# Kernel tuning notes

Measured on AMD Instinct MI355X. Metric: run time of the kernel, lower is better.

The kernel has to match this reference:

```python
import jax, jax.numpy as jnp
import numpy as np

N_NODES = 100000
N_EDGES = 640000
IN_DIM = 128
HID_DIM = 256
N_CLASS = 40
K = 3  # propagation steps


def setup_inputs() -> dict:
    key = jax.random.key(0)
    ks = jax.random.split(key, 5)
    feats = jax.random.normal(ks[0], (N_NODES, IN_DIM), dtype=jnp.float32)
    src = jax.random.randint(ks[1], (N_EDGES,), 0, N_NODES, dtype=jnp.int32)
    dst = jax.random.randint(ks[2], (N_EDGES,), 0, N_NODES, dtype=jnp.int32)
    W1 = jax.random.normal(ks[3], (IN_DIM, HID_DIM), dtype=jnp.float32) * (1.0 / np.sqrt(IN_DIM))
    b1 = jnp.zeros((HID_DIM,), dtype=jnp.float32)
    W2 = jax.random.normal(ks[4], (HID_DIM, N_CLASS), dtype=jnp.float32) * (1.0 / np.sqrt(HID_DIM))
    b2 = jnp.zeros((N_CLASS,), dtype=jnp.float32)
    return {"feats": feats, "src": src, "dst": dst, "W1": W1, "b1": b1, "W2": W2, "b2": b2}


def _grand_conv(feats, src, dst, order):
    # symmetric normalization: norm = in_deg^{-1/2} (clamped at 1)
    deg = jax.ops.segment_sum(jnp.ones_like(dst, dtype=feats.dtype), dst, num_segments=N_NODES)
    norm = jnp.clip(deg, 1.0) ** -0.5  # [N]
    w = (norm[src] * norm[dst])[:, None]  # [E, 1] edge weights (u_mul_v)
    x = feats
    y = feats
    for _ in range(order):
        # u_mul_e gather-multiply, then scatter-sum into dst (SpMM)
        x = jax.ops.segment_sum(x[src] * w, dst, num_segments=N_NODES)
        y = y + x
    return y / (order + 1)


def reference(feats, src, dst, W1, b1, W2, b2):
    h = _grand_conv(feats, src, dst, K)           # [N, IN_DIM]
    h = jax.nn.relu(h @ W1 + b1)                  # [N, HID_DIM]
    logits = h @ W2 + b2                          # [N, N_CLASS]
    return jax.nn.log_softmax(logits, axis=-1)
```

## Files before the change

kernel.cpp:

```cpp
#include <hip/hip_runtime.h>

#define NN 100000
#define NE 640000
#define IND 128
#define HD 256
#define NC 40
#define MT 64
#define HPAD 264
#define LPAD 52
#define NB 196
#define CAP 5120
#define EPB 2500
#define SGRID 2048

typedef unsigned short u16;
typedef unsigned int u32;
typedef __attribute__((ext_vector_type(8))) short bf16x8;
typedef __attribute__((ext_vector_type(4))) float f32x4;

__device__ __forceinline__ float bf2f(u16 u) {
    union { u32 i; float f; } c; c.i = ((u32)u) << 16; return c.f;
}
__device__ __forceinline__ u16 f2bf(float f) {
    union { float f; u32 i; } c; c.f = f;
    u32 i = c.i;
    return (u16)((i + 0x7FFFu + ((i >> 16) & 1u)) >> 16);
}
__device__ __forceinline__ float rfl_f(float v) {
    return __int_as_float(__builtin_amdgcn_readfirstlane(__float_as_int(v)));
}
__device__ __forceinline__ int wave_incl_scan(int v, int lane) {
    #pragma unroll
    for (int off = 1; off < 64; off <<= 1) {
        int t = __shfl_up(v, off);
        if (lane >= off) v += t;
    }
    return v;
}

__global__ __launch_bounds__(256) void prep_k(
    const float* __restrict__ W1, const float* __restrict__ W2,
    u16* __restrict__ pw1, u16* __restrict__ pw2)
{
    const int gtid = blockIdx.x * 256 + threadIdx.x;
    if (gtid < 4096) {
        int lane = gtid & 63, fid = gtid >> 6;
        int ks = fid & 3, ct = fid >> 2;
        int quad = lane >> 4, m = lane & 15;
        int n = ct * 16 + m;
        u16* o = pw1 + (size_t)gtid * 8;
        #pragma unroll
        for (int j = 0; j < 8; j++) o[j] = f2bf(W1[(ks * 32 + quad * 8 + j) * HD + n]);
    } else if (gtid < 4096 + 1536) {
        int idx = gtid - 4096;
        int lane = idx & 63, fid = idx >> 6;
        int ks = fid & 7, ct = fid >> 3;
        int quad = lane >> 4, m = lane & 15;
        int n = ct * 16 + m;
        u16* o = pw2 + (size_t)idx * 8;
        #pragma unroll
        for (int j = 0; j < 8; j++)
            o[j] = (n < NC) ? f2bf(W2[(ks * 32 + quad * 8 + j) * NC + n]) : (u16)0;
    }
}

__global__ __launch_bounds__(256) void bin_k(
    const int* __restrict__ src, const int* __restrict__ dst,
    int* __restrict__ gcur, u32* __restrict__ ebuf)
{
    __shared__ int cnt[NB], cur[NB], rdest[NB];
    __shared__ u32 vals[EPB];
    const int tid = threadIdx.x;
    const int e0 = blockIdx.x * EPB;

    if (tid < NB) cnt[tid] = 0;
    __syncthreads();
    for (int i = tid; i < EPB; i += 256)
        atomicAdd(&cnt[dst[e0 + i] >> 9], 1);
    __syncthreads();
    if (tid < 64) {
        int carry = 0;
        #pragma unroll
        for (int c = 0; c < 4; c++) {
            const int idx = c * 64 + tid;
            const int v = (idx < NB) ? cnt[idx] : 0;
            const int incl = wave_incl_scan(v, tid);
            if (idx < NB) cur[idx] = carry + incl - v;
            carry += __shfl(incl, 63);
        }
    }
    __syncthreads();
    for (int i = tid; i < EPB; i += 256) {
        const int s = src[e0 + i], d = dst[e0 + i];
        const int b = d >> 9;
        const int slot = atomicAdd(&cur[b], 1);
        vals[slot] = ((u32)(d & 511) << 17) | (u32)s;
    }
    __syncthreads();
    if (tid < NB) {
        const int c = cnt[tid];
        int st = 0;
        if (c > 0) st = atomicAdd(&gcur[tid], c);
        rdest[tid] = (st + c <= CAP) ? st : -1;
    }
    __syncthreads();
    if (tid < NB) {
        const int c = cnt[tid];
        const int st = rdest[tid];
        if (c > 0 && st >= 0) {
            const int lo = cur[tid] - c;
            u32* o = ebuf + (size_t)tid * CAP + st;
            for (int k = 0; k < c; k++) o[k] = vals[lo + k];
        }
    }
}

__global__ __launch_bounds__(256) void build_k(
    const int* __restrict__ gcur, u32* __restrict__ ebuf,
    int2* __restrict__ rb, float* __restrict__ norm, float* __restrict__ invn)
{
    __shared__ int rowcnt[512], rowoff[512], csum[8];
    __shared__ u32 evals[CAP];
    const int tid = threadIdx.x;
    const int b = blockIdx.x;
    const int bB = b * CAP;
    const int r0 = b * 512;
    const int nb = min(__builtin_amdgcn_readfirstlane(gcur[b]), CAP);

    rowcnt[tid] = 0; rowcnt[256 + tid] = 0;
    __syncthreads();
    for (int i = tid; i < nb; i += 256) {
        const u32 v = ebuf[bB + i];
        evals[i] = v;
        atomicAdd(&rowcnt[(v >> 17) & 511], 1);
    }
    __syncthreads();
    {
        const int w = tid >> 6, lane = tid & 63;
        #pragma unroll
        for (int r = 0; r < 2; r++) {
            const int c = r * 4 + w;
            const int v = rowcnt[c * 64 + lane];
            const int incl = wave_incl_scan(v, lane);
            rowoff[c * 64 + lane] = incl - v;
            if (lane == 63) csum[c] = incl;
        }
        __syncthreads();
        if (tid == 0) {
            int run = 0;
            #pragma unroll
            for (int c = 0; c < 8; c++) { const int t = csum[c]; csum[c] = run; run += t; }
        }
        __syncthreads();
        #pragma unroll
        for (int r = 0; r < 2; r++) {
            const int c = r * 4 + w;
            rowoff[c * 64 + lane] += csum[c];
        }
    }
    __syncthreads();
    #pragma unroll
    for (int r = 0; r < 2; r++) {
        const int idx = r * 256 + tid;
        const int row = r0 + idx;
        if (row < NN) {
            const int deg = rowcnt[idx];
            const int base = bB + rowoff[idx];
            rb[row] = make_int2(base, base + deg);
            const float dc = fmaxf((float)deg, 1.0f);
            norm[row] = rsqrtf(dc);
            invn[row] = sqrtf(dc);
        }
    }
    __syncthreads();
    for (int i = tid; i < nb; i += 256) {
        const u32 v = evals[i];
        const int rl = (v >> 17) & 511;
        const int pos = atomicAdd(&rowoff[rl], 1);
        ebuf[bB + pos] = v & 0x1FFFFu;
    }
}

__global__ __launch_bounds__(256) void conv_k(
    const float4* __restrict__ feats4, const float* __restrict__ norm,
    uint2* __restrict__ zF2, uint2* __restrict__ zA2, uint2* __restrict__ zB2)
{
    const int gtid = blockIdx.x * 256 + threadIdx.x, gsz = gridDim.x * 256;
    if (gtid < 96) {
        const int which = gtid >> 5, idx = gtid & 31;
        uint2* b = (which == 0) ? zF2 : (which == 1) ? zA2 : zB2;
        b[(size_t)NN * 32 + idx] = make_uint2(0u, 0u);
    }
    for (int i = gtid; i < NN * (IND / 4); i += gsz) {
        const float4 v = feats4[i];
        const float n = norm[i >> 5];
        uint2 o;
        o.x = (u32)f2bf(v.x * n) | ((u32)f2bf(v.y * n) << 16);
        o.y = (u32)f2bf(v.z * n) | ((u32)f2bf(v.w * n) << 16);
        zF2[i] = o;
    }
}

template <int LAST>
__global__ __launch_bounds__(256) void spmm_k(
    const u32* __restrict__ x, u32* __restrict__ xnext,
    const u32* __restrict__ x0, const u32* __restrict__ x1,
    const int2* __restrict__ rb, const int* __restrict__ csr,
    const float* __restrict__ norm, const float* __restrict__ invn)
{
    const int lane = threadIdx.x & 63;
    int wid = (blockIdx.x * 256 + threadIdx.x) >> 6;
    wid = __builtin_amdgcn_readfirstlane(wid);
    const int nw = SGRID * 4;

    for (int row = wid; row < NN; row += nw) {
        const int2 be = rb[row];
        const int beg = __builtin_amdgcn_readfirstlane(be.x);
        const int end = __builtin_amdgcn_readfirstlane(be.y);
        const float n = rfl_f(norm[row]);

        float a0 = 0.f, a1 = 0.f;
        for (int b = beg; b < end; b += 8) {
            int sN[8];
            #pragma unroll
            for (int j = 0; j < 8; j++) {
                const int ee = b + j;
                const int c = csr[ee];
                int s = __builtin_amdgcn_readfirstlane(c);
                if (ee >= end) s = NN;
                sN[j] = s;
            }
            u32 u[8];
            #pragma unroll
            for (int j = 0; j < 8; j++) {
                const u32* rp = x + ((size_t)sN[j] << 6);
                u[j] = rp[lane];
            }
            #pragma unroll
            for (int j = 0; j < 8; j++) {
                a0 += __int_as_float((int)(u[j] << 16));
                a1 += __int_as_float((int)(u[j] & 0xFFFF0000u));
            }
        }

        const size_t ri = (size_t)row * 64 + lane;
        u32 o;
        if (!LAST) {
            const float n2 = n * n;
            o = (u32)f2bf(a0 * n2) | ((u32)f2bf(a1 * n2) << 16);
        } else {
            const float inv = rfl_f(invn[row]);
            const u32 v0 = x0[ri];
            const u32 v1 = x1[ri];
            const u32 v2 = x[ri];
            const float s0 = (bf2f((u16)(v0 & 0xFFFFu)) + bf2f((u16)(v1 & 0xFFFFu))
                            + bf2f((u16)(v2 & 0xFFFFu))) * inv + a0 * n;
            const float s1 = (bf2f((u16)(v0 >> 16)) + bf2f((u16)(v1 >> 16))
                            + bf2f((u16)(v2 >> 16))) * inv + a1 * n;
            o = (u32)f2bf(s0 * 0.25f) | ((u32)f2bf(s1 * 0.25f) << 16);
        }
        xnext[ri] = o;
    }
}

__global__ __launch_bounds__(256, 4) void mlp_mfma_k(
    const u16* __restrict__ ys, const u16* __restrict__ pw1,
    const float* __restrict__ B1, const u16* __restrict__ pw2,
    const float* __restrict__ B2, float* __restrict__ out, int N)
{
    __shared__ __align__(16) u16 h_s[MT * HPAD];
    const int t = threadIdx.x;
    const int w = t >> 6, lane = t & 63;
    const int quad = lane >> 4, m = lane & 15;
    const int node0 = blockIdx.x * MT;
    float* const lw = (float*)((char*)h_s + (size_t)w * 16 * HPAD * 2);

    int nodeA = node0 + w * 16 + m;
    if (nodeA > N - 1) nodeA = N - 1;
    bf16x8 av[4];
    #pragma unroll
    for (int ks = 0; ks < 4; ks++)
        av[ks] = *(const bf16x8*)(ys + (size_t)nodeA * IND + ks * 32 + quad * 8);

    const u16* const pwl = pw1 + (size_t)lane * 8;
    bf16x8 wb[3][4];
    #pragma unroll
    for (int ks = 0; ks < 4; ks++) {
        wb[0][ks] = *(const bf16x8*)(pwl + (size_t)((0 * 4 + ks) * 64) * 8);
        wb[1][ks] = *(const bf16x8*)(pwl + (size_t)((1 * 4 + ks) * 64) * 8);
    }
    #pragma unroll
    for (int ct = 0; ct < 16; ct++) {
        if (ct + 2 < 16) {
            const int ns = (ct + 2) % 3;
            #pragma unroll
            for (int ks = 0; ks < 4; ks++)
                wb[ns][ks] = *(const bf16x8*)(pwl + (size_t)(((ct + 2) * 4 + ks) * 64) * 8);
        }
        const int cs = ct % 3;
        f32x4 acc = { 0.f, 0.f, 0.f, 0.f };
        #pragma unroll
        for (int ks = 0; ks < 4; ks++)
            acc = __builtin_amdgcn_mfma_f32_16x16x32_bf16(av[ks], wb[cs][ks], acc, 0, 0, 0);
        const float b1c = B1[ct * 16 + m];
        #pragma unroll
        for (int r = 0; r < 4; r++) {
            const float hv = fmaxf(acc[r] + b1c, 0.0f);
            h_s[(w * 16 + quad * 4 + r) * HPAD + ct * 16 + m] = f2bf(hv);
        }
    }

    const u16* const pw2l = pw2 + (size_t)lane * 8;
    f32x4 acc2[3];
    #pragma unroll
    for (int ct = 0; ct < 3; ct++) acc2[ct] = (f32x4){ 0.f, 0.f, 0.f, 0.f };
    bf16x8 w2[3][3];
    #pragma unroll
    for (int ct = 0; ct < 3; ct++) {
        w2[0][ct] = *(const bf16x8*)(pw2l + (size_t)((ct * 8 + 0) * 64) * 8);
        w2[1][ct] = *(const bf16x8*)(pw2l + (size_t)((ct * 8 + 1) * 64) * 8);
    }
    #pragma unroll
    for (int ks = 0; ks < 8; ks++) {
        if (ks + 2 < 8) {
            const int ns = (ks + 2) % 3;
            #pragma unroll
            for (int ct = 0; ct < 3; ct++)
                w2[ns][ct] = *(const bf16x8*)(pw2l + (size_t)((ct * 8 + ks + 2) * 64) * 8);
        }
        const int cs = ks % 3;
        const bf16x8 a = *(const bf16x8*)&h_s[(w * 16 + m) * HPAD + ks * 32 + quad * 8];
        #pragma unroll
        for (int ct = 0; ct < 3; ct++)
            acc2[ct] = __builtin_amdgcn_mfma_f32_16x16x32_bf16(a, w2[cs][ct], acc2[ct], 0, 0, 0);
    }
    #pragma unroll
    for (int ct = 0; ct < 3; ct++) {
        const int cg = ct * 16 + m;
        const float b2c = (cg < NC) ? B2[cg] : 0.0f;
        #pragma unroll
        for (int r = 0; r < 4; r++)
            lw[(quad * 4 + r) * LPAD + cg] = acc2[ct][r] + b2c;
    }
    __syncthreads();

    if (t < MT) {
        const int node = node0 + t;
        if (node < N) {
            const float* ln = (const float*)((const char*)h_s + (size_t)(t >> 4) * 16 * HPAD * 2)
                              + (t & 15) * LPAD;
            float mx = -1e30f;
            #pragma unroll
            for (int c = 0; c < NC; c++) mx = fmaxf(mx, ln[c]);
            float s = 0.0f;
            #pragma unroll
            for (int c = 0; c < NC; c++) s += __expf(ln[c] - mx);
            const float lse = mx + __logf(s);
            float4* o = (float4*)(out + (size_t)node * NC);
            #pragma unroll
            for (int c4 = 0; c4 < NC / 4; c4++) {
                float4 v;
                v.x = ln[c4 * 4 + 0] - lse;
                v.y = ln[c4 * 4 + 1] - lse;
                v.z = ln[c4 * 4 + 2] - lse;
                v.w = ln[c4 * 4 + 3] - lse;
                o[c4] = v;
            }
        }
    }
}

extern "C" void kernel_launch(void* const* d_in, const int* in_sizes, int n_in,
                              void* d_out, int out_size, void* d_ws, size_t ws_size,
                              hipStream_t stream) {
    const float* feats = (const float*)d_in[0];
    const int* src = (const int*)d_in[1];
    const int* dst = (const int*)d_in[2];
    const float* W1 = (const float*)d_in[3];
    const float* B1 = (const float*)d_in[4];
    const float* W2 = (const float*)d_in[5];
    const float* B2 = (const float*)d_in[6];
    float* out = (float*)d_out;

    char* base = (char*)d_ws;
    size_t off = 0;
    auto alloc = [&](size_t bytes) -> void* {
        void* p = base + off;
        off += (bytes + 255) & ~(size_t)255;
        return p;
    };
    int*   gcur = (int*)  alloc((size_t)NB * 4);
    float* norm = (float*)alloc((size_t)NN * 4);
    float* invn = (float*)alloc((size_t)NN * 4);
    int2*  rb   = (int2*) alloc((size_t)NN * 8);
    u32*   ebuf = (u32*)  alloc(((size_t)NB * CAP + 64) * 4);
    u16*   pw1  = (u16*)  alloc((size_t)16 * 4 * 64 * 8 * 2);
    u16*   pw2  = (u16*)  alloc((size_t)3 * 8 * 64 * 8 * 2);
    u32*   zF   = (u32*)  alloc((size_t)(NN + 1) * (IND / 2) * 4);
    u32*   zA   = (u32*)  alloc((size_t)(NN + 1) * (IND / 2) * 4);
    u32*   zB   = (u32*)  alloc((size_t)(NN + 1) * (IND / 2) * 4);
    u32*   ys   = (u32*)  alloc((size_t)NN * (IND / 2) * 4);

    hipMemsetAsync(gcur, 0, 1024, stream);

    prep_k<<<22, 256, 0, stream>>>(W1, W2, pw1, pw2);
    bin_k<<<256, 256, 0, stream>>>(src, dst, gcur, ebuf);
    build_k<<<NB, 256, 0, stream>>>(gcur, ebuf, rb, norm, invn);
    conv_k<<<2048, 256, 0, stream>>>((const float4*)feats, norm,
                                     (uint2*)zF, (uint2*)zA, (uint2*)zB);

    spmm_k<0><<<SGRID, 256, 0, stream>>>(zF, zA, nullptr, nullptr, rb, (const int*)ebuf, norm, invn);
    spmm_k<0><<<SGRID, 256, 0, stream>>>(zA, zB, nullptr, nullptr, rb, (const int*)ebuf, norm, invn);
    spmm_k<1><<<SGRID, 256, 0, stream>>>(zB, ys, zF, zA, rb, (const int*)ebuf, norm, invn);

    const int mgrid = (NN + MT - 1) / MT;
    mlp_mfma_k<<<mgrid, 256, 0, stream>>>((const u16*)ys, pw1, B1, pw2, B2, out, NN);
}
```

Baseline: 249.3 us.

## Split first MLP GEMM across waves by output columns instead of rows

Each wave previously computed all 256 hidden columns for its own 16 rows, loading the full W1 from global per wave. Now each wave loads all 64 rows of A and computes only its 4 column tiles, so each W1 fragment is reused across 4 MFMAs and per-wave weight traffic is cut to a quarter. A __syncthreads is added because the second GEMM now reads h rows written by other waves. The cost is 4x more A-register loads per wave and higher register pressure from 16 A fragments and 4 accumulators.

```diff
diff --git a/kernel.cpp b/kernel.cpp
--- a/kernel.cpp
+++ b/kernel.cpp
@@ -275,40 +275,52 @@
     const int node0 = blockIdx.x * MT;
     float* const lw = (float*)((char*)h_s + (size_t)w * 16 * HPAD * 2);
 
-    int nodeA = node0 + w * 16 + m;
-    if (nodeA > N - 1) nodeA = N - 1;
-    bf16x8 av[4];
+    bf16x8 av[4][4];
+    #pragma unroll
+    for (int g = 0; g < 4; g++) {
+        int node = node0 + g * 16 + m;
+        if (node > N - 1) node = N - 1;
+        #pragma unroll
+        for (int ks = 0; ks < 4; ks++)
+            av[g][ks] = *(const bf16x8*)(ys + (size_t)node * IND + ks * 32 + quad * 8);
+    }
+
+    const u16* const pwl = pw1 + (size_t)lane * 8;
+    const int ct0 = w * 4;
+    bf16x8 wb[2][4];
     #pragma unroll
     for (int ks = 0; ks < 4; ks++)
-        av[ks] = *(const bf16x8*)(ys + (size_t)nodeA * IND + ks * 32 + quad * 8);
-
-    const u16* const pwl = pw1 + (size_t)lane * 8;
-    bf16x8 wb[3][4];
-    #pragma unroll
-    for (int ks = 0; ks < 4; ks++) {
-        wb[0][ks] = *(const bf16x8*)(pwl + (size_t)((0 * 4 + ks) * 64) * 8);
-        wb[1][ks] = *(const bf16x8*)(pwl + (size_t)((1 * 4 + ks) * 64) * 8);
-    }
-    #pragma unroll
-    for (int ct = 0; ct < 16; ct++) {
-        if (ct + 2 < 16) {
-            const int ns = (ct + 2) % 3;
+        wb[0][ks] = *(const bf16x8*)(pwl + (size_t)((ct0 * 4 + ks) * 64) * 8);
+    #pragma unroll
+    for (int ct2 = 0; ct2 < 4; ct2++) {
+        const int ct = ct0 + ct2;
+        if (ct2 + 1 < 4) {
             #pragma unroll
             for (int ks = 0; ks < 4; ks++)
-                wb[ns][ks] = *(const bf16x8*)(pwl + (size_t)(((ct + 2) * 4 + ks) * 64) * 8);
-        }
-        const int cs = ct % 3;
-        f32x4 acc = { 0.f, 0.f, 0.f, 0.f };
-        #pragma unroll
-        for (int ks = 0; ks < 4; ks++)
-            acc = __builtin_amdgcn_mfma_f32_16x16x32_bf16(av[ks], wb[cs][ks], acc, 0, 0, 0);
+                wb[(ct2 + 1) & 1][ks] =
+                    *(const bf16x8*)(pwl + (size_t)(((ct + 1) * 4 + ks) * 64) * 8);
+        }
+        const int cs = ct2 & 1;
+        f32x4 acc[4];
+        #pragma unroll
+        for (int g = 0; g < 4; g++) acc[g] = (f32x4){ 0.f, 0.f, 0.f, 0.f };
+        #pragma unroll
+        for (int ks = 0; ks < 4; ks++) {
+            #pragma unroll
+            for (int g = 0; g < 4; g++)
+                acc[g] = __builtin_amdgcn_mfma_f32_16x16x32_bf16(av[g][ks], wb[cs][ks], acc[g], 0, 0, 0);
+        }
         const float b1c = B1[ct * 16 + m];
         #pragma unroll
-        for (int r = 0; r < 4; r++) {
-            const float hv = fmaxf(acc[r] + b1c, 0.0f);
-            h_s[(w * 16 + quad * 4 + r) * HPAD + ct * 16 + m] = f2bf(hv);
-        }
-    }
+        for (int g = 0; g < 4; g++) {
+            #pragma unroll
+            for (int r = 0; r < 4; r++) {
+                const float hv = fmaxf(acc[g][r] + b1c, 0.0f);
+                h_s[(g * 16 + quad * 4 + r) * HPAD + ct * 16 + m] = f2bf(hv);
+            }
+        }
+    }
+    __syncthreads();
 
     const u16* const pw2l = pw2 + (size_t)lane * 8;
     f32x4 acc2[3];
```

New measurement: 247.0 us. Within noise of the previous version (-0.9%).
